# Kernel tuning notes

Measured on AMD Instinct MI355X. Metric: run time of the kernel, lower is better.

The kernel has to match this reference:

```python
import jax, jax.numpy as jnp
import numpy as np

C, H, W = 512, 192, 192  # feature map dims; 3x3 patches at stride 3 (non-overlapping)


def setup_inputs() -> dict:
    key = jax.random.key(0)
    k1, k2 = jax.random.split(key)
    model_resp = jax.random.normal(k1, (1, C, H, W), dtype=jnp.float32)
    style_resp = jax.random.normal(k2, (1, C, H, W), dtype=jnp.float32)
    return {"model_resp": model_resp, "style_resp": style_resp}


def _unfold3(x):
    # torch.nn.Unfold(kernel=3, stride=3) on (1, C, H, W) -> (C*9, L) after the
    # module's view(patch_count, patch_size) (note: rows are feature channels,
    # columns are spatial locations, matching the original code's dim order).
    _, c, h, w = x.shape
    p = x[0].reshape(c, h // 3, 3, w // 3, 3)          # (c, ph, kh, pw, kw)
    p = p.transpose(0, 2, 4, 1, 3)                      # (c, kh, kw, ph, pw)
    return p.reshape(c * 9, (h // 3) * (w // 3))        # (A, L)


def reference(model_resp, style_resp):
    img = _unfold3(model_resp)                          # (A, L)
    sty = _unfold3(style_resp)                          # (A, L)
    img_norm = 1.0 / jnp.linalg.norm(img, axis=1)       # (A,)
    sty_norm = 1.0 / jnp.linalg.norm(sty, axis=1)       # (A,)
    S = img @ sty.T                                     # (A, A), S[i,j] = img_i . sty_j
    # Faithful to torch: expand(A, A) of a 1-D tensor broadcasts along dim 0,
    # i.e. multiplies COLUMNS by the normalizer vector.
    S1 = S * img_norm[None, :]
    S2 = S1.T * sty_norm[None, :]                       # S2[i,j] = img_norm[i]*sty_norm[j]*(img_j . sty_i)
    nearest = jnp.argmax(S2, axis=0)                    # (A,) int
    max_sim = jnp.max(S2, axis=0)                       # (A,) float (the online-max values)
    return nearest, max_sim
```

## Files before the change

kernel.cpp:

```cpp
#include <hip/hip_runtime.h>
#include <hip/hip_bf16.h>
#include <hip/hip_fp16.h>

#define A_DIM 4608
#define L_DIM 4096
#define CH    512
#define H_DIM 192
#define W_DIM 192

#define BM 128
#define BN 128
#define BK 32
#define NS (L_DIM / BK)

#define CPB 32

typedef _Float16 half8 __attribute__((ext_vector_type(8)));
typedef float   floatx4 __attribute__((ext_vector_type(4)));
typedef float   floatx16 __attribute__((ext_vector_type(16)));

__global__ __launch_bounds__(256) void prep_kernel(
    const float* __restrict__ x0, const float* __restrict__ x1,
    _Float16* __restrict__ Uhi0, _Float16* __restrict__ Ulo0,
    _Float16* __restrict__ Uhi1, _Float16* __restrict__ Ulo1,
    float* __restrict__ ss0, float* __restrict__ ss1) {
  const int which = blockIdx.z;
  const float* __restrict__ x = which ? x1 : x0;
  _Float16* __restrict__ Uhi = which ? Uhi1 : Uhi0;
  _Float16* __restrict__ Ulo = which ? Ulo1 : Ulo0;
  float* __restrict__ ssg = which ? ss1 : ss0;

  const int ph = blockIdx.y;
  const int c0 = blockIdx.x * CPB;
  const int abase = blockIdx.x * (CPB * 9);

  __shared__ _Float16 sHi[CPB * 9 * 8 * 8];
  __shared__ _Float16 sLo[CPB * 9 * 8 * 8];
  __shared__ float ssb[CPB * 9];

  const int t = threadIdx.x;
  for (int a = t; a < CPB * 9; a += 256) ssb[a] = 0.f;
  __syncthreads();

  const int c_l = t >> 3;
  const int s = t & 7;
  const float* __restrict__ rowbase =
      x + ((size_t)(c0 + c_l) * H_DIM + 3 * ph) * W_DIM + s * 24;
  float ssp[9] = {0.f, 0.f, 0.f, 0.f, 0.f, 0.f, 0.f, 0.f, 0.f};

#pragma unroll
  for (int kh = 0; kh < 3; ++kh) {
    const float* __restrict__ rp = rowbase + kh * W_DIM;
    floatx4 v4[6];
#pragma unroll
    for (int i = 0; i < 6; ++i) v4[i] = *(const floatx4*)(rp + i * 4);
    half8 hv[3], lv[3];
#pragma unroll
    for (int i = 0; i < 6; ++i)
#pragma unroll
      for (int j = 0; j < 4; ++j) {
        const int m = i * 4 + j;
        const int kw = m % 3, e = m / 3;
        const float v = v4[i][j];
        ssp[kh * 3 + kw] += v * v;
        const _Float16 h = (_Float16)v;
        hv[kw][e] = h;
        lv[kw][e] = (_Float16)(v - (float)h);
      }
#pragma unroll
    for (int kw = 0; kw < 3; ++kw) {
      const int a_l = c_l * 9 + kh * 3 + kw;
      const int addr = (a_l * 8 + (s ^ (a_l & 7))) * 8;
      *(half8*)&sHi[addr] = hv[kw];
      *(half8*)&sLo[addr] = lv[kw];
    }
  }
#pragma unroll
  for (int q = 0; q < 9; ++q) atomicAdd(&ssb[c_l * 9 + q], ssp[q]);
  __syncthreads();

#pragma unroll
  for (int i = 0; i < 9; ++i) {
    const int idx = i * 256 + t;
    const int c8 = idx / 288;
    const int a_l = idx - c8 * 288;
    const int addr = (a_l * 8 + (c8 ^ (a_l & 7))) * 8;
    const size_t g = ((size_t)(ph * 8 + c8) * A_DIM + abase + a_l) * 8;
    *(half8*)&Uhi[g] = *(const half8*)&sHi[addr];
    *(half8*)&Ulo[g] = *(const half8*)&sLo[addr];
  }
  for (int a = t; a < CPB * 9; a += 256) atomicAdd(&ssg[abase + a], ssb[a]);
}

#define GLDS(g, l)                                                          \
  __builtin_amdgcn_global_load_lds(                                        \
      (const __attribute__((address_space(1))) void*)(g),                   \
      (__attribute__((address_space(3))) void*)(l), 16, 0, 0)

__global__ __launch_bounds__(256, 2) void gemm_max_kernel(
    const _Float16* __restrict__ Shi, const _Float16* __restrict__ Slo,
    const _Float16* __restrict__ Ihi, const _Float16* __restrict__ Ilo,
    const float* __restrict__ img_ss,
    unsigned long long* __restrict__ packed) {
  __shared__ _Float16 sm[2][4][4 * 128 * 8];

  const int t = threadIdx.x;
  const int lane = t & 63, wv = t >> 6;
  const int wvr = wv >> 1, wvc = wv & 1;
  const int id = blockIdx.x;
  int bx, by;
  if (id < 1152) {
    const int g = id / 288, r = id - g * 288;
    by = r >> 3; bx = g * 8 + (r & 7);
  } else {
    const int r = id - 1152;
    by = r >> 2; bx = 32 + (r & 3);
  }
  const int row0 = by * BM;
  const int col0 = bx * BN;
  const int l31 = lane & 31, hs = lane >> 5;

  floatx16 acc[2][2];
#pragma unroll
  for (int rf = 0; rf < 2; ++rf)
#pragma unroll
    for (int cf = 0; cf < 2; ++cf) acc[rf][cf] = (floatx16)0.f;

  const size_t CH8 = (size_t)A_DIM * 8;
  const size_t so = (size_t)(t & 127) * 8 + (size_t)(t >> 7) * CH8;
  const _Float16* __restrict__ pAh = Shi + (size_t)row0 * 8 + so;
  const _Float16* __restrict__ pAl = Slo + (size_t)row0 * 8 + so;
  const _Float16* __restrict__ pBh = Ihi + (size_t)col0 * 8 + so;
  const _Float16* __restrict__ pBl = Ilo + (size_t)col0 * 8 + so;
  const int dl = t * 8;

#define ISSUE(b, off)                                      \
  do {                                                     \
    GLDS(pAh + (off),           &sm[b][0][dl]);            \
    GLDS(pAh + (off) + 2 * CH8, &sm[b][0][dl + 2048]);     \
    GLDS(pAl + (off),           &sm[b][1][dl]);            \
    GLDS(pAl + (off) + 2 * CH8, &sm[b][1][dl + 2048]);     \
    GLDS(pBh + (off),           &sm[b][2][dl]);            \
    GLDS(pBh + (off) + 2 * CH8, &sm[b][2][dl + 2048]);     \
    GLDS(pBl + (off),           &sm[b][3][dl]);            \
    GLDS(pBl + (off) + 2 * CH8, &sm[b][3][dl + 2048]);     \
  } while (0)

  ISSUE(0, 0);

  for (int ks = 0; ks < NS; ++ks) {
    const int cur = ks & 1;
    if (ks + 1 < NS) {
      ISSUE(1 - cur, (size_t)(ks + 1) * 4 * CH8);
      asm volatile("s_waitcnt vmcnt(8)" ::: "memory");
    } else {
      asm volatile("s_waitcnt vmcnt(0)" ::: "memory");
    }
    asm volatile("s_barrier" ::: "memory");

#pragma unroll
    for (int kk = 0; kk < 2; ++kk) {
      const int kc = kk * 2 + hs;
      half8 ah[2], al[2], bh[2], bl[2];
#pragma unroll
      for (int rf = 0; rf < 2; ++rf) {
        const int idx = (kc * 128 + wvr * 64 + rf * 32 + l31) * 8;
        ah[rf] = *(const half8*)&sm[cur][0][idx];
        al[rf] = *(const half8*)&sm[cur][1][idx];
      }
#pragma unroll
      for (int cf = 0; cf < 2; ++cf) {
        const int idx = (kc * 128 + wvc * 64 + cf * 32 + l31) * 8;
        bh[cf] = *(const half8*)&sm[cur][2][idx];
        bl[cf] = *(const half8*)&sm[cur][3][idx];
      }
#pragma unroll
      for (int rf = 0; rf < 2; ++rf)
#pragma unroll
        for (int cf = 0; cf < 2; ++cf)
          acc[rf][cf] = __builtin_amdgcn_mfma_f32_32x32x16_f16(
              ah[rf], bh[cf], acc[rf][cf], 0, 0, 0);
#pragma unroll
      for (int rf = 0; rf < 2; ++rf)
#pragma unroll
        for (int cf = 0; cf < 2; ++cf)
          acc[rf][cf] = __builtin_amdgcn_mfma_f32_32x32x16_f16(
              ah[rf], bl[cf], acc[rf][cf], 0, 0, 0);
#pragma unroll
      for (int rf = 0; rf < 2; ++rf)
#pragma unroll
        for (int cf = 0; cf < 2; ++cf)
          acc[rf][cf] = __builtin_amdgcn_mfma_f32_32x32x16_f16(
              al[rf], bh[cf], acc[rf][cf], 0, 0, 0);
    }
    asm volatile("s_barrier" ::: "memory");
  }

  float nrv[2][16];
#pragma unroll
  for (int rf = 0; rf < 2; ++rf) {
    const int base_i = row0 + wvr * 64 + rf * 32 + 4 * hs;
#pragma unroll
    for (int g = 0; g < 4; ++g) {
      const floatx4 s4 = *(const floatx4*)&img_ss[base_i + 8 * g];
#pragma unroll
      for (int r = 0; r < 4; ++r) nrv[rf][g * 4 + r] = 1.0f / sqrtf(s4[r]);
    }
  }
#pragma unroll
  for (int cf = 0; cf < 2; ++cf) {
    const int j = col0 + wvc * 64 + cf * 32 + l31;
    float best = -3.4e38f;
    int bi = 0x7FFFFFFF;
#pragma unroll
    for (int rf = 0; rf < 2; ++rf) {
      const int base_i = row0 + wvr * 64 + rf * 32 + 4 * hs;
#pragma unroll
      for (int g = 0; g < 4; ++g)
#pragma unroll
        for (int r = 0; r < 4; ++r) {
          const int i = base_i + 8 * g + r;
          const float v = acc[rf][cf][g * 4 + r] * nrv[rf][g * 4 + r];
          if (v > best) { best = v; bi = i; }
        }
    }
    const float ov = __shfl_xor(best, 32, 64);
    const int oi = __shfl_xor(bi, 32, 64);
    if (ov > best || (ov == best && oi < bi)) { best = ov; bi = oi; }
    if (hs == 0) {
      const unsigned u = __float_as_uint(best);
      const unsigned key = (u & 0x80000000u) ? ~u : (u | 0x80000000u);
      const unsigned long long pk =
          ((unsigned long long)key << 32) | (unsigned)(~(unsigned)bi);
      atomicMax(&packed[j], pk);
    }
  }
}

__global__ __launch_bounds__(256) void finalize_kernel(
    const unsigned long long* __restrict__ packed,
    const float* __restrict__ sty_ss, float* __restrict__ out) {
  const int j = blockIdx.x * 256 + threadIdx.x;
  if (j >= A_DIM) return;
  const unsigned long long p = packed[j];
  const unsigned key = (unsigned)(p >> 32);
  const unsigned u = (key & 0x80000000u) ? (key ^ 0x80000000u) : ~key;
  const float v = __uint_as_float(u);
  const int idx = (int)(~(unsigned)(p & 0xFFFFFFFFu));
  out[j] = (float)idx;
  out[A_DIM + j] = v * (1.0f / sqrtf(sty_ss[j]));
}

extern "C" void kernel_launch(void* const* d_in, const int* in_sizes, int n_in,
                              void* d_out, int out_size, void* d_ws, size_t ws_size,
                              hipStream_t stream) {
  const float* model = (const float*)d_in[0];
  const float* style = (const float*)d_in[1];
  float* out = (float*)d_out;
  char* ws = (char*)d_ws;

  const size_t usz = (size_t)A_DIM * L_DIM * 2;
  _Float16* img_hi = (_Float16*)(ws);
  _Float16* img_lo = (_Float16*)(ws + usz);
  _Float16* sty_hi = (_Float16*)(ws + 2 * usz);
  _Float16* sty_lo = (_Float16*)(ws + 3 * usz);
  float* img_ss = (float*)(ws + 4 * usz);
  float* sty_ss = img_ss + A_DIM;
  unsigned long long* packed = (unsigned long long*)(img_ss + 2 * A_DIM);

  hipMemsetAsync(img_ss, 0, (size_t)A_DIM * 16, stream);
  prep_kernel<<<dim3(CH / CPB, H_DIM / 3, 2), 256, 0, stream>>>(
      model, style, img_hi, img_lo, sty_hi, sty_lo, img_ss, sty_ss);
  gemm_max_kernel<<<dim3(1296), 256, 0, stream>>>(
      sty_hi, sty_lo, img_hi, img_lo, img_ss, packed);
  finalize_kernel<<<18, 256, 0, stream>>>(packed, sty_ss, out);
}
```

Measured before the change: 725.6 us.

## Halve GEMM K-tile to shrink LDS and raise occupancy; shuffle-reduce norms in prep

```diff
diff --git a/kernel.cpp b/kernel.cpp
--- a/kernel.cpp
+++ b/kernel.cpp
@@ -10,7 +10,7 @@
 
 #define BM 128
 #define BN 128
-#define BK 32
+#define BK 16
 #define NS (L_DIM / BK)
 
 #define CPB 32
@@ -36,11 +36,8 @@
 
   __shared__ _Float16 sHi[CPB * 9 * 8 * 8];
   __shared__ _Float16 sLo[CPB * 9 * 8 * 8];
-  __shared__ float ssb[CPB * 9];
 
   const int t = threadIdx.x;
-  for (int a = t; a < CPB * 9; a += 256) ssb[a] = 0.f;
-  __syncthreads();
 
   const int c_l = t >> 3;
   const int s = t & 7;
@@ -76,7 +73,13 @@
     }
   }
 #pragma unroll
-  for (int q = 0; q < 9; ++q) atomicAdd(&ssb[c_l * 9 + q], ssp[q]);
+  for (int q = 0; q < 9; ++q) {
+    float v = ssp[q];
+    v += __shfl_down(v, 4, 8);
+    v += __shfl_down(v, 2, 8);
+    v += __shfl_down(v, 1, 8);
+    if (s == 0) atomicAdd(&ssg[abase + c_l * 9 + q], v);
+  }
   __syncthreads();
 
 #pragma unroll
@@ -89,7 +92,6 @@
     *(half8*)&Uhi[g] = *(const half8*)&sHi[addr];
     *(half8*)&Ulo[g] = *(const half8*)&sLo[addr];
   }
-  for (int a = t; a < CPB * 9; a += 256) atomicAdd(&ssg[abase + a], ssb[a]);
 }
 
 #define GLDS(g, l)                                                          \
@@ -97,12 +99,12 @@
       (const __attribute__((address_space(1))) void*)(g),                   \
       (__attribute__((address_space(3))) void*)(l), 16, 0, 0)
 
-__global__ __launch_bounds__(256, 2) void gemm_max_kernel(
+__global__ __launch_bounds__(256, 4) void gemm_max_kernel(
     const _Float16* __restrict__ Shi, const _Float16* __restrict__ Slo,
     const _Float16* __restrict__ Ihi, const _Float16* __restrict__ Ilo,
     const float* __restrict__ img_ss,
     unsigned long long* __restrict__ packed) {
-  __shared__ _Float16 sm[2][4][4 * 128 * 8];
+  __shared__ _Float16 sm[2][8192];
 
   const int t = threadIdx.x;
   const int lane = t & 63, wv = t >> 6;
@@ -127,23 +129,16 @@
     for (int cf = 0; cf < 2; ++cf) acc[rf][cf] = (floatx16)0.f;
 
   const size_t CH8 = (size_t)A_DIM * 8;
-  const size_t so = (size_t)(t & 127) * 8 + (size_t)(t >> 7) * CH8;
-  const _Float16* __restrict__ pAh = Shi + (size_t)row0 * 8 + so;
-  const _Float16* __restrict__ pAl = Slo + (size_t)row0 * 8 + so;
-  const _Float16* __restrict__ pBh = Ihi + (size_t)col0 * 8 + so;
-  const _Float16* __restrict__ pBl = Ilo + (size_t)col0 * 8 + so;
+  const size_t aOff = (size_t)(t >> 7) * CH8 + (size_t)(row0 + (t & 127)) * 8;
+  const size_t bOff = (size_t)(t >> 7) * CH8 + (size_t)(col0 + (t & 127)) * 8;
   const int dl = t * 8;
 
-#define ISSUE(b, off)                                      \
-  do {                                                     \
-    GLDS(pAh + (off),           &sm[b][0][dl]);            \
-    GLDS(pAh + (off) + 2 * CH8, &sm[b][0][dl + 2048]);     \
-    GLDS(pAl + (off),           &sm[b][1][dl]);            \
-    GLDS(pAl + (off) + 2 * CH8, &sm[b][1][dl + 2048]);     \
-    GLDS(pBh + (off),           &sm[b][2][dl]);            \
-    GLDS(pBh + (off) + 2 * CH8, &sm[b][2][dl + 2048]);     \
-    GLDS(pBl + (off),           &sm[b][3][dl]);            \
-    GLDS(pBl + (off) + 2 * CH8, &sm[b][3][dl + 2048]);     \
+#define ISSUE(b, koff)                              \
+  do {                                              \
+    GLDS(Shi + (koff) + aOff, &sm[b][dl]);          \
+    GLDS(Slo + (koff) + aOff, &sm[b][2048 + dl]);   \
+    GLDS(Ihi + (koff) + bOff, &sm[b][4096 + dl]);   \
+    GLDS(Ilo + (koff) + bOff, &sm[b][6144 + dl]);   \
   } while (0)
 
   ISSUE(0, 0);
@@ -151,48 +146,46 @@
   for (int ks = 0; ks < NS; ++ks) {
     const int cur = ks & 1;
     if (ks + 1 < NS) {
-      ISSUE(1 - cur, (size_t)(ks + 1) * 4 * CH8);
-      asm volatile("s_waitcnt vmcnt(8)" ::: "memory");
+      ISSUE(1 - cur, (size_t)(ks + 1) * 2 * CH8);
+      asm volatile("s_waitcnt vmcnt(4)" ::: "memory");
     } else {
       asm volatile("s_waitcnt vmcnt(0)" ::: "memory");
     }
     asm volatile("s_barrier" ::: "memory");
 
-#pragma unroll
-    for (int kk = 0; kk < 2; ++kk) {
-      const int kc = kk * 2 + hs;
-      half8 ah[2], al[2], bh[2], bl[2];
-#pragma unroll
-      for (int rf = 0; rf < 2; ++rf) {
-        const int idx = (kc * 128 + wvr * 64 + rf * 32 + l31) * 8;
-        ah[rf] = *(const half8*)&sm[cur][0][idx];
-        al[rf] = *(const half8*)&sm[cur][1][idx];
-      }
-#pragma unroll
-      for (int cf = 0; cf < 2; ++cf) {
-        const int idx = (kc * 128 + wvc * 64 + cf * 32 + l31) * 8;
-        bh[cf] = *(const half8*)&sm[cur][2][idx];
-        bl[cf] = *(const half8*)&sm[cur][3][idx];
-      }
-#pragma unroll
-      for (int rf = 0; rf < 2; ++rf)
-#pragma unroll
-        for (int cf = 0; cf < 2; ++cf)
-          acc[rf][cf] = __builtin_amdgcn_mfma_f32_32x32x16_f16(
-              ah[rf], bh[cf], acc[rf][cf], 0, 0, 0);
-#pragma unroll
-      for (int rf = 0; rf < 2; ++rf)
-#pragma unroll
-        for (int cf = 0; cf < 2; ++cf)
-          acc[rf][cf] = __builtin_amdgcn_mfma_f32_32x32x16_f16(
-              ah[rf], bl[cf], acc[rf][cf], 0, 0, 0);
-#pragma unroll
-      for (int rf = 0; rf < 2; ++rf)
-#pragma unroll
-        for (int cf = 0; cf < 2; ++cf)
-          acc[rf][cf] = __builtin_amdgcn_mfma_f32_32x32x16_f16(
-              al[rf], bh[cf], acc[rf][cf], 0, 0, 0);
-    }
+    const _Float16* __restrict__ S = &sm[cur][0];
+    half8 ah[2], al[2], bh[2], bl[2];
+#pragma unroll
+    for (int rf = 0; rf < 2; ++rf) {
+      const int idx = (hs * 128 + wvr * 64 + rf * 32 + l31) * 8;
+      ah[rf] = *(const half8*)&S[idx];
+      al[rf] = *(const half8*)&S[2048 + idx];
+    }
+#pragma unroll
+    for (int cf = 0; cf < 2; ++cf) {
+      const int idx = (hs * 128 + wvc * 64 + cf * 32 + l31) * 8;
+      bh[cf] = *(const half8*)&S[4096 + idx];
+      bl[cf] = *(const half8*)&S[6144 + idx];
+    }
+#pragma unroll
+    for (int rf = 0; rf < 2; ++rf)
+#pragma unroll
+      for (int cf = 0; cf < 2; ++cf)
+        acc[rf][cf] = __builtin_amdgcn_mfma_f32_32x32x16_f16(
+            ah[rf], bh[cf], acc[rf][cf], 0, 0, 0);
+#pragma unroll
+    for (int rf = 0; rf < 2; ++rf)
+#pragma unroll
+      for (int cf = 0; cf < 2; ++cf)
+        acc[rf][cf] = __builtin_amdgcn_mfma_f32_32x32x16_f16(
+            ah[rf], bl[cf], acc[rf][cf], 0, 0, 0);
+#pragma unroll
+    for (int rf = 0; rf < 2; ++rf)
+#pragma unroll
+      for (int cf = 0; cf < 2; ++cf)
+        acc[rf][cf] = __builtin_amdgcn_mfma_f32_32x32x16_f16(
+            al[rf], bh[cf], acc[rf][cf], 0, 0, 0);
+
     asm volatile("s_barrier" ::: "memory");
   }
 
@@ -201,10 +194,10 @@
   for (int rf = 0; rf < 2; ++rf) {
     const int base_i = row0 + wvr * 64 + rf * 32 + 4 * hs;
 #pragma unroll
-    for (int g = 0; g < 4; ++g) {
-      const floatx4 s4 = *(const floatx4*)&img_ss[base_i + 8 * g];
-#pragma unroll
-      for (int r = 0; r < 4; ++r) nrv[rf][g * 4 + r] = 1.0f / sqrtf(s4[r]);
+    for (int g2 = 0; g2 < 4; ++g2) {
+      const floatx4 s4 = *(const floatx4*)&img_ss[base_i + 8 * g2];
+#pragma unroll
+      for (int r2 = 0; r2 < 4; ++r2) nrv[rf][g2 * 4 + r2] = 1.0f / sqrtf(s4[r2]);
     }
   }
 #pragma unroll
@@ -216,11 +209,11 @@
     for (int rf = 0; rf < 2; ++rf) {
       const int base_i = row0 + wvr * 64 + rf * 32 + 4 * hs;
 #pragma unroll
-      for (int g = 0; g < 4; ++g)
-#pragma unroll
-        for (int r = 0; r < 4; ++r) {
-          const int i = base_i + 8 * g + r;
-          const float v = acc[rf][cf][g * 4 + r] * nrv[rf][g * 4 + r];
+      for (int g2 = 0; g2 < 4; ++g2)
+#pragma unroll
+        for (int r2 = 0; r2 < 4; ++r2) {
+          const int i = base_i + 8 * g2 + r2;
+          const float v = acc[rf][cf][g2 * 4 + r2] * nrv[rf][g2 * 4 + r2];
           if (v > best) { best = v; bi = i; }
         }
     }
@@ -271,7 +264,7 @@
   hipMemsetAsync(img_ss, 0, (size_t)A_DIM * 16, stream);
   prep_kernel<<<dim3(CH / CPB, H_DIM / 3, 2), 256, 0, stream>>>(
       model, style, img_hi, img_lo, sty_hi, sty_lo, img_ss, sty_ss);
-  gemm_max_kernel<<<dim3(1296), 256, 0, stream>>>(
+  gemm_max_kernel<<<dim3((A_DIM / BM) * (A_DIM / BN)), 256, 0, stream>>>(
       sty_hi, sty_lo, img_hi, img_lo, img_ss, packed);
   finalize_kernel<<<18, 256, 0, stream>>>(packed, sty_ss, out);
 }
```

New measurement: 708.0 us. 2.4% less time.
